# Performance work log

Hardware: AMD Instinct MI355X
Metric: run time of the kernel (lower is better)

The kernel has to match this reference:

```python
import jax, jax.numpy as jnp
import numpy as np

HEADS = 16
PHI = (1.0 + np.sqrt(5.0)) / 2.0


def setup_inputs() -> dict:
    key = jax.random.key(0)
    k1, k2, k3, k4 = jax.random.split(key, 4)
    B, L, D = 2, 2048, 1024
    x = jax.random.normal(k1, (B, L, D), dtype=jnp.float32)
    # nn.Linear(dim, 3*dim, bias=False): store as [D, 3D] for x @ W
    w_qkv = jax.random.normal(k2, (D, 3 * D), dtype=jnp.float32) * (D ** -0.5)
    w_proj = jax.random.normal(k3, (D, D), dtype=jnp.float32) * (D ** -0.5)
    b_proj = jax.random.normal(k4, (D,), dtype=jnp.float32) * 0.01
    return {"x": x, "w_qkv": w_qkv, "w_proj": w_proj, "b_proj": b_proj}


def phi_bias(L):
    # pos[i] = (i * phi) mod 1 ; bias = log(exp(-|pos_i - pos_j|) + 1e-8)
    pos = (jnp.arange(L, dtype=jnp.float32) * PHI) % 1.0
    dist = jnp.abs(pos[:, None] - pos[None, :])  # [L, L]
    return jnp.log(jnp.exp(-dist) + 1e-8)


def reference(x, w_qkv, w_proj, b_proj):
    B, L, D = x.shape
    H = HEADS
    Dh = D // H
    scale = Dh ** -0.5
    qkv = (x @ w_qkv).reshape(B, L, 3, H, Dh)
    q = jnp.transpose(qkv[:, :, 0], (0, 2, 1, 3))  # [B, H, L, Dh]
    k = jnp.transpose(qkv[:, :, 1], (0, 2, 1, 3))
    v = jnp.transpose(qkv[:, :, 2], (0, 2, 1, 3))
    attn = jnp.einsum("bhid,bhjd->bhij", q, k) * scale  # [B, H, L, L]
    attn = attn + phi_bias(L)[None, None]  # additive phi-distance bias
    attn = jax.nn.softmax(attn, axis=-1)
    out = jnp.einsum("bhij,bhjd->bhid", attn, v)  # [B, H, L, Dh]
    out = jnp.transpose(out, (0, 2, 1, 3)).reshape(B, L, D)
    return out @ w_proj + b_proj
```

## Files before the change

kernel.cpp:

```cpp
#include <hip/hip_runtime.h>
#include <math.h>


typedef _Float16 f16;
typedef _Float16 f16x4 __attribute__((ext_vector_type(4)));
typedef _Float16 f16x8 __attribute__((ext_vector_type(8)));
typedef float f32x4 __attribute__((ext_vector_type(4)));

#define MFMA32(a, b, c) __builtin_amdgcn_mfma_f32_16x16x32_f16(a, b, c, 0, 0, 0)

static constexpr int Bsz = 2, Lseq = 2048, Dm = 1024, H = 16, Dh = 64;
static constexpr int Mtot = Bsz * Lseq;
static constexpr int NQKV = 3 * Dm;
static constexpr float PHI_F = 1.61803398874989484820f;
static constexpr float LOG2E = 1.44269504088896f;
static constexpr float QS = 0.125f * LOG2E;
static constexpr float CSTEP = 0.55417527999932633f;

__device__ __forceinline__ void load16_to_lds(const f16* g, f16* l) {
  __builtin_amdgcn_global_load_lds(
      (const __attribute__((address_space(1))) unsigned int*)g,
      (__attribute__((address_space(3))) unsigned int*)l, 16, 0, 0);
}

__global__ __launch_bounds__(256) void cast_f32_f16(const float* __restrict__ in,
                                                    f16* __restrict__ out, int n) {
  int i = (blockIdx.x * 256 + threadIdx.x) * 4;
  if (i < n) {
    float4 v = *reinterpret_cast<const float4*>(in + i);
    f16 t[4] = {(f16)v.x, (f16)v.y, (f16)v.z, (f16)v.w};
    *reinterpret_cast<uint2*>(out + i) = *reinterpret_cast<uint2*>(t);
  }
}

__global__ __launch_bounds__(256) void transpose_cast(const float* __restrict__ in,
                                                      f16* __restrict__ out,
                                                      int K, int N) {
  __shared__ float tile[32][33];
  int n0 = blockIdx.x * 32, k0 = blockIdx.y * 32;
  int tx = threadIdx.x & 31, ty = threadIdx.x >> 5;
#pragma unroll
  for (int r = 0; r < 32; r += 8)
    tile[ty + r][tx] = in[(size_t)(k0 + ty + r) * N + n0 + tx];
  __syncthreads();
#pragma unroll
  for (int r = 0; r < 32; r += 8)
    out[(size_t)(n0 + ty + r) * K + k0 + tx] = (f16)tile[tx][ty + r];
}

template <int MODE>
__global__ __launch_bounds__(256) void gemm_f16(
    const f16* __restrict__ A, const f16* __restrict__ Bt,
    int M, int N, int K,
    f16* __restrict__ qb, f16* __restrict__ kb, f16* __restrict__ vb,
    float* __restrict__ out, const float* __restrict__ bias) {
  constexpr int BM = (MODE == 0) ? 128 : 64;
  constexpr int MI = BM / 32;
  constexpr int AI = BM / 32;
  __shared__ f16 As[BM * 64];
  __shared__ f16 Bs[128 * 64];

  int tid = threadIdx.x;
  int wave = tid >> 6, lane = tid & 63;
  int quad = lane >> 4, l16 = lane & 15;
  int wm = (wave >> 1) * (MI * 16), wn = (wave & 1) * 64;

  int lid = blockIdx.x;
  int xcd = lid & 7, t = lid >> 3;
  int m0, n0;
  if (MODE == 0) {
    int mg = xcd >> 1, ng = xcd & 1;
    m0 = (mg * 8 + t / 12) * 128;
    n0 = (ng * 12 + t % 12) * 128;
  } else {
    m0 = (xcd * 8 + (t >> 3)) * 64;
    n0 = (t & 7) * 128;
  }

  const int gu = (lane & 7) ^ (lane >> 3);
  const f16* gA[AI];
  f16* lA[AI];
#pragma unroll
  for (int i = 0; i < AI; i++) {
    int it = wave * AI + i;
    gA[i] = A + (size_t)(m0 + it * 8 + (lane >> 3)) * K + gu * 8;
    lA[i] = As + it * 512;
  }
  const f16* gB[4];
  f16* lB[4];
#pragma unroll
  for (int i = 0; i < 4; i++) {
    int it = wave * 4 + i;
    gB[i] = Bt + (size_t)(n0 + it * 8 + (lane >> 3)) * K + gu * 8;
    lB[i] = Bs + it * 512;
  }

  f32x4 acc[MI][4] = {};

  for (int k0 = 0; k0 < K; k0 += 64) {
#pragma unroll
    for (int i = 0; i < AI; i++) load16_to_lds(gA[i] + k0, lA[i]);
#pragma unroll
    for (int i = 0; i < 4; i++) load16_to_lds(gB[i] + k0, lB[i]);
    __syncthreads();
#pragma unroll
    for (int s = 0; s < 2; s++) {
      f16x8 a[MI], b[4];
#pragma unroll
      for (int i = 0; i < MI; i++) {
        int row = wm + i * 16 + l16;
        a[i] = *reinterpret_cast<const f16x8*>(
            As + row * 64 + (((s * 4 + quad) ^ (l16 & 7)) * 8));
      }
#pragma unroll
      for (int j = 0; j < 4; j++) {
        int row = wn + j * 16 + l16;
        b[j] = *reinterpret_cast<const f16x8*>(
            Bs + row * 64 + (((s * 4 + quad) ^ (l16 & 7)) * 8));
      }
#pragma unroll
      for (int i = 0; i < MI; i++)
#pragma unroll
        for (int j = 0; j < 4; j++)
          acc[i][j] = MFMA32(a[i], b[j], acc[i][j]);
    }
    __syncthreads();
  }

#pragma unroll
  for (int i = 0; i < MI; i++) {
#pragma unroll
    for (int j = 0; j < 4; j++) {
      int n = n0 + wn + j * 16 + l16;
      if (MODE == 0) {
        int ty = n >> 10;
        int df = n & 1023;
        int h = df >> 6, dh = df & 63;
        int mb = m0 + wm + i * 16 + quad * 4;
        int b = mb >> 11, l = mb & 2047;
        int bhh = b * H + h;
        if (ty == 2) {
          int jj = l & 63;
          int jh = jj >> 5, rem = jj & 31;
          int qd = (rem & 15) >> 2;
          int e0 = (rem >= 16) ? 4 : 0;
          f16x4 tmp;
#pragma unroll
          for (int r = 0; r < 4; r++) tmp[r] = (f16)acc[i][j][r];
          *reinterpret_cast<uint2*>(
              vb + (size_t)bhh * (Dh * Lseq) + (l >> 6) * 4096 + dh * 64 +
              (jh * 4 + qd) * 8 + e0) = *reinterpret_cast<uint2*>(&tmp);
        } else {
          size_t idx = (((size_t)bhh) * Lseq + l) * Dh + dh;
          if (ty == 0) {
#pragma unroll
            for (int r = 0; r < 4; r++)
              qb[idx + (size_t)r * Dh] = (f16)(acc[i][j][r] * QS);
          } else {
#pragma unroll
            for (int r = 0; r < 4; r++)
              kb[idx + (size_t)r * Dh] = (f16)acc[i][j][r];
          }
        }
      } else {
#pragma unroll
        for (int r = 0; r < 4; r++) {
          int m = m0 + wm + i * 16 + quad * 4 + r;
          out[(size_t)m * N + n] = acc[i][j][r] + bias[n];
        }
      }
    }
  }
}

__global__ __launch_bounds__(256, 4) void attn_kernel(
    const f16* __restrict__ qb,
    const f16* __restrict__ kb,
    const f16* __restrict__ vb,
    f16* __restrict__ ctx) {
  __shared__ __align__(16) unsigned char smem[16640];
  f16* Ks = (f16*)smem;
  f16* Vs = (f16*)(smem + 8192);

  int bh = blockIdx.y;
  int q0 = blockIdx.x * 64;
  int tid = threadIdx.x, wave = tid >> 6, lane = tid & 63;
  int quad = lane >> 4, l16 = lane & 15;
  int jhalf = wave >> 1, qhalf = wave & 1;

  f16x8 qfrag[2][2];
  float pq[2];
#pragma unroll
  for (int set = 0; set < 2; set++) {
    int q = q0 + qhalf * 32 + set * 16 + l16;
    const f16* Qrow = qb + ((size_t)bh * Lseq + q) * Dh;
    qfrag[set][0] = *reinterpret_cast<const f16x8*>(Qrow + quad * 8);
    qfrag[set][1] = *reinterpret_cast<const f16x8*>(Qrow + 32 + quad * 8);
    pq[set] = fmodf((float)q * PHI_F, 1.0f);
  }

  float pk[2][4];
#pragma unroll
  for (int jb = 0; jb < 2; jb++)
#pragma unroll
    for (int r = 0; r < 4; r++) {
      int j = jhalf * 32 + jb * 16 + quad * 4 + r;
      pk[jb][r] = fmodf((float)j * PHI_F, 1.0f);
    }

  const f16* Kbh = kb + (size_t)bh * Lseq * Dh;
  const f16* Vbh = vb + (size_t)bh * Dh * Lseq;
  const int gu = (lane & 7) ^ (lane >> 3);
  const f16* gK[2];
  const f16* gV[2];
  f16* lK[2];
  f16* lV[2];
#pragma unroll
  for (int i = 0; i < 2; i++) {
    int g8 = (wave * 2 + i) * 8 + (lane >> 3);
    gK[i] = Kbh + (size_t)g8 * Dh + gu * 8;
    gV[i] = Vbh + (size_t)g8 * 64 + gu * 8;
    lK[i] = Ks + (wave * 2 + i) * 512;
    lV[i] = Vs + (wave * 2 + i) * 512;
  }

  const f16 one = (f16)1.0f;
  const f16x8 ones8 = {one, one, one, one, one, one, one, one};

  f32x4 acc_o[2][4] = {};
  f32x4 acc_l[2] = {};

  for (int j0 = 0; j0 < Lseq; j0 += 64) {
    __syncthreads();
#pragma unroll
    for (int i = 0; i < 2; i++) {
      load16_to_lds(gK[i] + (size_t)j0 * Dh, lK[i]);
      load16_to_lds(gV[i] + (size_t)j0 * 64, lV[i]);
    }
    __syncthreads();

    f32x4 accs[2][2] = {};
#pragma unroll
    for (int s = 0; s < 2; s++)
#pragma unroll
      for (int jb = 0; jb < 2; jb++) {
        f16x8 kf = *reinterpret_cast<const f16x8*>(
            Ks + (jhalf * 32 + jb * 16 + l16) * 64 + (((s * 4 + quad) ^ (l16 & 7)) * 8));
        accs[0][jb] = MFMA32(kf, qfrag[0][s], accs[0][jb]);
        accs[1][jb] = MFMA32(kf, qfrag[1][s], accs[1][jb]);
      }

    f16x8 pf8[2];
#pragma unroll
    for (int set = 0; set < 2; set++) {
#pragma unroll
      for (int jb = 0; jb < 2; jb++) {
        float p[4];
#pragma unroll
        for (int r = 0; r < 4; r++) {
          float d = pq[set] - pk[jb][r];
          float arg = fmaf(-LOG2E, fabsf(d), accs[set][jb][r]);
          p[r] = __builtin_amdgcn_exp2f(arg);
        }
        auto lo = __builtin_amdgcn_cvt_pkrtz(p[0], p[1]);
        auto hi = __builtin_amdgcn_cvt_pkrtz(p[2], p[3]);
        pf8[set][jb * 4 + 0] = lo[0];
        pf8[set][jb * 4 + 1] = lo[1];
        pf8[set][jb * 4 + 2] = hi[0];
        pf8[set][jb * 4 + 3] = hi[1];
      }
      acc_l[set] = MFMA32(ones8, pf8[set], acc_l[set]);
    }
#pragma unroll
    for (int jb = 0; jb < 2; jb++)
#pragma unroll
      for (int r = 0; r < 4; r++)
        pk[jb][r] = __builtin_amdgcn_fractf(pk[jb][r] + CSTEP);

#pragma unroll
    for (int dblk = 0; dblk < 4; dblk++) {
      int row = dblk * 16 + l16;
      f16x8 va = *reinterpret_cast<const f16x8*>(
          Vs + row * 64 + (((jhalf * 4 + quad) ^ (l16 & 7)) * 8));
      acc_o[0][dblk] = MFMA32(va, pf8[0], acc_o[0][dblk]);
      acc_o[1][dblk] = MFMA32(va, pf8[1], acc_o[1][dblk]);
    }
  }

  __syncthreads();
  float* Oex = (float*)smem;
  float* Lex = (float*)(smem + 16384);
  if (jhalf == 1) {
#pragma unroll
    for (int set = 0; set < 2; set++) {
#pragma unroll
      for (int dblk = 0; dblk < 4; dblk++)
#pragma unroll
        for (int r = 0; r < 4; r++)
          Oex[(((qhalf * 2 + set) * 4 + dblk) * 16 + quad * 4 + r) * 16 + l16] =
              acc_o[set][dblk][r];
      if (quad == 0) Lex[(qhalf * 2 + set) * 16 + l16] = acc_l[set][0];
    }
  }
  __syncthreads();
  if (jhalf == 0) {
    int b = bh >> 4, h = bh & 15;
#pragma unroll
    for (int set = 0; set < 2; set++) {
      float ltot = acc_l[set][0] + Lex[(qhalf * 2 + set) * 16 + l16];
      float inv = 1.0f / ltot;
      int q = q0 + qhalf * 32 + set * 16 + l16;
      f16* crow = ctx + (size_t)(b * Lseq + q) * Dm + h * 64;
#pragma unroll
      for (int dblk = 0; dblk < 4; dblk++) {
        f16x4 o;
#pragma unroll
        for (int r = 0; r < 4; r++) {
          float full = acc_o[set][dblk][r] +
              Oex[(((qhalf * 2 + set) * 4 + dblk) * 16 + quad * 4 + r) * 16 + l16];
          o[r] = (f16)(full * inv);
        }
        *reinterpret_cast<uint2*>(crow + dblk * 16 + quad * 4) =
            *reinterpret_cast<uint2*>(&o);
      }
    }
  }
}

extern "C" void kernel_launch(void* const* d_in, const int* in_sizes, int n_in,
                              void* d_out, int out_size, void* d_ws, size_t ws_size,
                              hipStream_t stream) {
  const float* x      = (const float*)d_in[0];
  const float* w_qkv  = (const float*)d_in[1];
  const float* w_proj = (const float*)d_in[2];
  const float* b_proj = (const float*)d_in[3];
  float* out = (float*)d_out;

  f16* xb    = (f16*)d_ws;
  f16* wqkvT = xb + (size_t)Mtot * Dm;
  f16* wpT   = wqkvT + (size_t)NQKV * Dm;
  f16* qb    = wpT + (size_t)Dm * Dm;
  f16* kb    = qb + (size_t)Bsz * H * Lseq * Dh;
  f16* vb    = kb + (size_t)Bsz * H * Lseq * Dh;
  f16* ctx   = vb + (size_t)Bsz * H * Lseq * Dh;

  cast_f32_f16<<<(Mtot * Dm) / (256 * 4), 256, 0, stream>>>(x, xb, Mtot * Dm);
  transpose_cast<<<dim3(NQKV / 32, Dm / 32), 256, 0, stream>>>(w_qkv, wqkvT, Dm, NQKV);
  transpose_cast<<<dim3(Dm / 32, Dm / 32), 256, 0, stream>>>(w_proj, wpT, Dm, Dm);

  gemm_f16<0><<<768, 256, 0, stream>>>(
      xb, wqkvT, Mtot, NQKV, Dm, qb, kb, vb, nullptr, nullptr);

  attn_kernel<<<dim3(Lseq / 64, Bsz * H), 256, 0, stream>>>(qb, kb, vb, ctx);

  gemm_f16<1><<<512, 256, 0, stream>>>(
      ctx, wpT, Mtot, Dm, Dm, nullptr, nullptr, nullptr, out, b_proj);
}
```

Before: 189.7 us.

## Fuse prep kernels and widen attention blocks to 128 queries with 8 waves

Result: faster. 180.8 us (-4.7%).

```diff
diff --git a/kernel.cpp b/kernel.cpp
--- a/kernel.cpp
+++ b/kernel.cpp
@@ -23,21 +23,32 @@
       (__attribute__((address_space(3))) unsigned int*)l, 16, 0, 0);
 }
 
-__global__ __launch_bounds__(256) void cast_f32_f16(const float* __restrict__ in,
-                                                    f16* __restrict__ out, int n) {
-  int i = (blockIdx.x * 256 + threadIdx.x) * 4;
-  if (i < n) {
-    float4 v = *reinterpret_cast<const float4*>(in + i);
+__global__ __launch_bounds__(256) void prep_fused(
+    const float* __restrict__ x, f16* __restrict__ xb,
+    const float* __restrict__ wqkv, f16* __restrict__ wqkvT,
+    const float* __restrict__ wproj, f16* __restrict__ wpT) {
+  __shared__ float tile[32][33];
+  int blk = blockIdx.x;
+  if (blk < 4096) {
+    int i = (blk * 256 + threadIdx.x) * 4;
+    float4 v = *reinterpret_cast<const float4*>(x + i);
     f16 t[4] = {(f16)v.x, (f16)v.y, (f16)v.z, (f16)v.w};
-    *reinterpret_cast<uint2*>(out + i) = *reinterpret_cast<uint2*>(t);
-  }
-}
-
-__global__ __launch_bounds__(256) void transpose_cast(const float* __restrict__ in,
-                                                      f16* __restrict__ out,
-                                                      int K, int N) {
-  __shared__ float tile[32][33];
-  int n0 = blockIdx.x * 32, k0 = blockIdx.y * 32;
+    *reinterpret_cast<uint2*>(xb + i) = *reinterpret_cast<uint2*>(t);
+    return;
+  }
+  const float* in;
+  f16* out;
+  int N, bx, by;
+  if (blk < 7168) {
+    int local = blk - 4096;
+    bx = local % 96; by = local / 96; N = NQKV;
+    in = wqkv; out = wqkvT;
+  } else {
+    int local = blk - 7168;
+    bx = local & 31; by = local >> 5; N = Dm;
+    in = wproj; out = wpT;
+  }
+  int n0 = bx * 32, k0 = by * 32;
   int tx = threadIdx.x & 31, ty = threadIdx.x >> 5;
 #pragma unroll
   for (int r = 0; r < 32; r += 8)
@@ -45,7 +56,7 @@
   __syncthreads();
 #pragma unroll
   for (int r = 0; r < 32; r += 8)
-    out[(size_t)(n0 + ty + r) * K + k0 + tx] = (f16)tile[tx][ty + r];
+    out[(size_t)(n0 + ty + r) * Dm + k0 + tx] = (f16)tile[tx][ty + r];
 }
 
 template <int MODE>
@@ -173,26 +184,28 @@
   }
 }
 
-__global__ __launch_bounds__(256, 4) void attn_kernel(
+__global__ __launch_bounds__(512, 4) void attn_kernel(
     const f16* __restrict__ qb,
     const f16* __restrict__ kb,
     const f16* __restrict__ vb,
     f16* __restrict__ ctx) {
-  __shared__ __align__(16) unsigned char smem[16640];
+  __shared__ __align__(16) unsigned char smem[33280];
   f16* Ks = (f16*)smem;
   f16* Vs = (f16*)(smem + 8192);
 
-  int bh = blockIdx.y;
-  int q0 = blockIdx.x * 64;
+  int id = blockIdx.x;
+  int bh = (id & 7) * 4 + ((id >> 3) >> 4);
+  int q0 = ((id >> 3) & 15) * 128;
+
   int tid = threadIdx.x, wave = tid >> 6, lane = tid & 63;
   int quad = lane >> 4, l16 = lane & 15;
-  int jhalf = wave >> 1, qhalf = wave & 1;
+  int jhalf = wave >> 2, qq = wave & 3;
 
   f16x8 qfrag[2][2];
   float pq[2];
 #pragma unroll
   for (int set = 0; set < 2; set++) {
-    int q = q0 + qhalf * 32 + set * 16 + l16;
+    int q = q0 + qq * 32 + set * 16 + l16;
     const f16* Qrow = qb + ((size_t)bh * Lseq + q) * Dh;
     qfrag[set][0] = *reinterpret_cast<const f16x8*>(Qrow + quad * 8);
     qfrag[set][1] = *reinterpret_cast<const f16x8*>(Qrow + 32 + quad * 8);
@@ -211,18 +224,11 @@
   const f16* Kbh = kb + (size_t)bh * Lseq * Dh;
   const f16* Vbh = vb + (size_t)bh * Dh * Lseq;
   const int gu = (lane & 7) ^ (lane >> 3);
-  const f16* gK[2];
-  const f16* gV[2];
-  f16* lK[2];
-  f16* lV[2];
-#pragma unroll
-  for (int i = 0; i < 2; i++) {
-    int g8 = (wave * 2 + i) * 8 + (lane >> 3);
-    gK[i] = Kbh + (size_t)g8 * Dh + gu * 8;
-    gV[i] = Vbh + (size_t)g8 * 64 + gu * 8;
-    lK[i] = Ks + (wave * 2 + i) * 512;
-    lV[i] = Vs + (wave * 2 + i) * 512;
-  }
+  int g8 = wave * 8 + (lane >> 3);
+  const f16* gK = Kbh + (size_t)g8 * Dh + gu * 8;
+  const f16* gV = Vbh + (size_t)g8 * 64 + gu * 8;
+  f16* lK = Ks + wave * 512;
+  f16* lV = Vs + wave * 512;
 
   const f16 one = (f16)1.0f;
   const f16x8 ones8 = {one, one, one, one, one, one, one, one};
@@ -232,11 +238,8 @@
 
   for (int j0 = 0; j0 < Lseq; j0 += 64) {
     __syncthreads();
-#pragma unroll
-    for (int i = 0; i < 2; i++) {
-      load16_to_lds(gK[i] + (size_t)j0 * Dh, lK[i]);
-      load16_to_lds(gV[i] + (size_t)j0 * 64, lV[i]);
-    }
+    load16_to_lds(gK + (size_t)j0 * Dh, lK);
+    load16_to_lds(gV + (size_t)j0 * 64, lV);
     __syncthreads();
 
     f32x4 accs[2][2] = {};
@@ -289,7 +292,7 @@
 
   __syncthreads();
   float* Oex = (float*)smem;
-  float* Lex = (float*)(smem + 16384);
+  float* Lex = (float*)(smem + 32768);
   if (jhalf == 1) {
 #pragma unroll
     for (int set = 0; set < 2; set++) {
@@ -297,9 +300,9 @@
       for (int dblk = 0; dblk < 4; dblk++)
 #pragma unroll
         for (int r = 0; r < 4; r++)
-          Oex[(((qhalf * 2 + set) * 4 + dblk) * 16 + quad * 4 + r) * 16 + l16] =
+          Oex[(((qq * 2 + set) * 4 + dblk) * 16 + quad * 4 + r) * 16 + l16] =
               acc_o[set][dblk][r];
-      if (quad == 0) Lex[(qhalf * 2 + set) * 16 + l16] = acc_l[set][0];
+      if (quad == 0) Lex[(qq * 2 + set) * 16 + l16] = acc_l[set][0];
     }
   }
   __syncthreads();
@@ -307,9 +310,9 @@
     int b = bh >> 4, h = bh & 15;
 #pragma unroll
     for (int set = 0; set < 2; set++) {
-      float ltot = acc_l[set][0] + Lex[(qhalf * 2 + set) * 16 + l16];
+      float ltot = acc_l[set][0] + Lex[(qq * 2 + set) * 16 + l16];
       float inv = 1.0f / ltot;
-      int q = q0 + qhalf * 32 + set * 16 + l16;
+      int q = q0 + qq * 32 + set * 16 + l16;
       f16* crow = ctx + (size_t)(b * Lseq + q) * Dm + h * 64;
 #pragma unroll
       for (int dblk = 0; dblk < 4; dblk++) {
@@ -317,7 +320,7 @@
 #pragma unroll
         for (int r = 0; r < 4; r++) {
           float full = acc_o[set][dblk][r] +
-              Oex[(((qhalf * 2 + set) * 4 + dblk) * 16 + quad * 4 + r) * 16 + l16];
+              Oex[(((qq * 2 + set) * 4 + dblk) * 16 + quad * 4 + r) * 16 + l16];
           o[r] = (f16)(full * inv);
         }
         *reinterpret_cast<uint2*>(crow + dblk * 16 + quad * 4) =
@@ -344,14 +347,12 @@
   f16* vb    = kb + (size_t)Bsz * H * Lseq * Dh;
   f16* ctx   = vb + (size_t)Bsz * H * Lseq * Dh;
 
-  cast_f32_f16<<<(Mtot * Dm) / (256 * 4), 256, 0, stream>>>(x, xb, Mtot * Dm);
-  transpose_cast<<<dim3(NQKV / 32, Dm / 32), 256, 0, stream>>>(w_qkv, wqkvT, Dm, NQKV);
-  transpose_cast<<<dim3(Dm / 32, Dm / 32), 256, 0, stream>>>(w_proj, wpT, Dm, Dm);
+  prep_fused<<<8192, 256, 0, stream>>>(x, xb, w_qkv, wqkvT, w_proj, wpT);
 
   gemm_f16<0><<<768, 256, 0, stream>>>(
       xb, wqkvT, Mtot, NQKV, Dm, qb, kb, vb, nullptr, nullptr);
 
-  attn_kernel<<<dim3(Lseq / 64, Bsz * H), 256, 0, stream>>>(qb, kb, vb, ctx);
+  attn_kernel<<<512, 512, 0, stream>>>(qb, kb, vb, ctx);
 
   gemm_f16<1><<<512, 256, 0, stream>>>(
       ctx, wpT, Mtot, Dm, Dm, nullptr, nullptr, nullptr, out, b_proj);
```
